# Kernel tuning notes

Measured on AMD Instinct MI355X. Metric: run time of the kernel, lower is better.

## Reference

```python
import jax, jax.numpy as jnp
import numpy as np

SR = 2  # sr_ratio

def _avgpool2x2(x):
    # x: [B,C,H,W] -> [B,C,H//2,W//2]
    B, C, H, W = x.shape
    return x.reshape(B, C, H // SR, SR, W // SR, SR).mean(axis=(3, 5))

def setup_inputs() -> dict:
    key = jax.random.key(0)
    ks = jax.random.split(key, 6)
    B, C, H, W = 8, 256, 64, 64
    d = C // 8
    sc_qk = 1.0 / np.sqrt(C)
    return {
        "x": jax.random.normal(ks[0], (B, C, H, W), jnp.float32),
        "wq": jax.random.normal(ks[1], (d, C), jnp.float32) * sc_qk,
        "wk": jax.random.normal(ks[2], (d, C), jnp.float32) * sc_qk,
        "wv": jax.random.normal(ks[3], (C, C), jnp.float32) * sc_qk,
        "wo": jax.random.normal(ks[4], (C, C), jnp.float32) * sc_qk,
        "gamma": jax.random.normal(ks[5], (1,), jnp.float32),
    }

def reference(x, wq, wk, wv, wo, gamma):
    B, C, H, W = x.shape
    N = H * W
    d = wq.shape[0]
    # q: conv1x1 then flatten+transpose -> [B, N, d]
    q = jnp.einsum('dc,bchw->bhwd', wq, x).reshape(B, N, d)
    # spatial reduction of K/V source
    x_kv = _avgpool2x2(x)
    Hk, Wk = x_kv.shape[2], x_kv.shape[3]
    Nk = Hk * Wk
    k = jnp.einsum('dc,bchw->bdhw', wk, x_kv).reshape(B, d, Nk)   # [B,d,Nk]
    v = jnp.einsum('oc,bchw->bohw', wv, x_kv).reshape(B, C, Nk)   # [B,C,Nk]
    # attn = softmax(q @ k / sqrt(d)) over Nk
    attn = jax.nn.softmax(jnp.einsum('bnd,bdm->bnm', q, k) / jnp.sqrt(jnp.float32(d)), axis=-1)
    # out = v @ attn^T -> [B,C,N]
    out = jnp.einsum('bcm,bnm->bcn', v, attn).reshape(B, C, H, W)
    out = jnp.einsum('oc,bchw->bohw', wo, out)
    return x + gamma[0] * out
```

## Files before the change

### kernel.cpp

```cpp
#include <hip/hip_runtime.h>

#define BB 8
#define CC 256
#define NN 4096
#define DD 32
#define NK 1024

typedef unsigned short u16;
typedef unsigned int   u32;
typedef __attribute__((ext_vector_type(8))) short bf16x8;
typedef __attribute__((ext_vector_type(4))) float f32x4;

#define MFMA16 __builtin_amdgcn_mfma_f32_16x16x32_bf16

#define OFF_WVO  0u
#define OFF_WQB  32768u
#define OFF_WKB  36864u
#define OFF_QF   40960u
#define OFF_KF   565248u
#define OFF_VOF  696320u

__device__ __forceinline__ u16 f2bf(float f) {
    u32 u = __float_as_uint(f);
    u += 0x7FFFu + ((u >> 16) & 1u);
    return (u16)(u >> 16);
}

__device__ __forceinline__ u32 cvt_pk_bf16(float lo, float hi) {
    u32 r;
    asm("v_cvt_pk_bf16_f32 %0, %1, %2" : "=v"(r) : "v"(lo), "v"(hi));
    return r;
}

__launch_bounds__(1024)
__global__ void wprep_kernel(const float* __restrict__ wq, const float* __restrict__ wk,
                             const float* __restrict__ wv, const float* __restrict__ wo,
                             u16* __restrict__ wqb, u16* __restrict__ wkb,
                             u16* __restrict__ wvob) {
    __shared__ float part[4][256];
    int o = blockIdx.x, t = threadIdx.x;
    int jq = t >> 8, c = t & 255;
    const float* wvp = wv + (size_t)(jq * 64) * CC + c;
    const float* wop = wo + o * CC + jq * 64;
    float acc = 0.f;
#pragma unroll 8
    for (int i = 0; i < 64; ++i)
        acc += wop[i] * wvp[(size_t)i * CC];
    part[jq][c] = acc;
    __syncthreads();
    if (t < 256)
        wvob[o * CC + t] = f2bf(part[0][t] + part[1][t] + part[2][t] + part[3][t]);
    if (o < 8) {
        const float QS = 0.17677669529663687f * 1.4426950408889634f;
        int id = o * 1024 + t;
        wqb[id] = f2bf(wq[id] * QS);
    } else if (o < 16) {
        int id = (o - 8) * 1024 + t;
        wkb[id] = f2bf(wk[id]);
    }
}

__launch_bounds__(256)
__global__ void proj_kernel(const float* __restrict__ x,
                            const u16* __restrict__ wqb, const u16* __restrict__ wkb,
                            const u16* __restrict__ wvob,
                            u16* __restrict__ qF, u16* __restrict__ kF,
                            u16* __restrict__ voF) {
    int t = threadIdx.x, w = t >> 6, l = t & 63, l15 = l & 15, lg = l >> 4;
    const f32x4 fz = {0.f, 0.f, 0.f, 0.f};

    if (blockIdx.x < 256) {
        __shared__ float xl[64 * 136];
        int b = blockIdx.x & 7, nb = blockIdx.x >> 3;
        int n0 = nb * 128;
        f32x4 acc[2][2];
        acc[0][0] = fz; acc[0][1] = fz; acc[1][0] = fz; acc[1][1] = fz;
        int cr = t >> 2, seg = (t & 3) * 32;
        for (int ch = 0; ch < 4; ++ch) {
            int c0 = ch * 64;
            const float* xs = x + ((size_t)(b * CC + c0 + cr)) * NN + n0 + seg;
#pragma unroll
            for (int p = 0; p < 8; ++p)
                *(float4*)&xl[cr * 136 + seg + p * 4] = *(const float4*)(xs + p * 4);
            __syncthreads();
#pragma unroll
            for (int ks = 0; ks < 2; ++ks) {
                int klo = ks * 32 + lg * 8;
#pragma unroll
                for (int i = 0; i < 2; ++i) {
                    int nl = w * 32 + i * 16 + l15;
                    float f0 = xl[(klo + 0) * 136 + nl];
                    float f1 = xl[(klo + 1) * 136 + nl];
                    float f2 = xl[(klo + 2) * 136 + nl];
                    float f3 = xl[(klo + 3) * 136 + nl];
                    float f4 = xl[(klo + 4) * 136 + nl];
                    float f5 = xl[(klo + 5) * 136 + nl];
                    float f6 = xl[(klo + 6) * 136 + nl];
                    float f7 = xl[(klo + 7) * 136 + nl];
                    union { u32 u[4]; bf16x8 v; } cv;
                    cv.u[0] = cvt_pk_bf16(f0, f1);
                    cv.u[1] = cvt_pk_bf16(f2, f3);
                    cv.u[2] = cvt_pk_bf16(f4, f5);
                    cv.u[3] = cvt_pk_bf16(f6, f7);
#pragma unroll
                    for (int dt = 0; dt < 2; ++dt) {
                        bf16x8 bq = *(const bf16x8*)(wqb + (size_t)(dt * 16 + l15) * CC + c0 + klo);
                        acc[i][dt] = MFMA16(cv.v, bq, acc[i][dt], 0, 0, 0);
                    }
                }
            }
            __syncthreads();
        }
        u16* outp = qF + (size_t)b * 256 * 512;
#pragma unroll
        for (int i = 0; i < 2; ++i)
#pragma unroll
            for (int dt = 0; dt < 2; ++dt)
#pragma unroll
                for (int r2 = 0; r2 < 4; ++r2) {
                    int tile = nb * 8 + w * 2 + i;
                    int dhi = dt * 2 + (l15 >> 3);
                    outp[((size_t)tile * 64 + dhi * 16 + lg * 4 + r2) * 8 + (l15 & 7)]
                        = f2bf(acc[i][dt][r2]);
                }
    } else {
        __shared__ u16 pl[64 * 42];
        int blk2 = blockIdx.x - 256;
        int b = blk2 & 7, hk = blk2 >> 3;
        f32x4 acck = fz;
        f32x4 accv[2][4];
#pragma unroll
        for (int mt = 0; mt < 2; ++mt)
#pragma unroll
            for (int ot = 0; ot < 4; ++ot) accv[mt][ot] = fz;

        int cr = t >> 2, w8 = (t & 3) * 8;
        for (int ch = 0; ch < 4; ++ch) {
            int c0 = ch * 64;
            const float* xs = x + ((size_t)(b * CC + c0 + cr)) * NN + (2 * hk) * 64 + w8 * 2;
            float4 A0 = *(const float4*)(xs +  0), A1 = *(const float4*)(xs +  4);
            float4 A2 = *(const float4*)(xs +  8), A3 = *(const float4*)(xs + 12);
            float4 B0 = *(const float4*)(xs + 64), B1 = *(const float4*)(xs + 68);
            float4 B2 = *(const float4*)(xs + 72), B3 = *(const float4*)(xs + 76);
            float p0 = 0.25f * (A0.x + A0.y + B0.x + B0.y);
            float p1 = 0.25f * (A0.z + A0.w + B0.z + B0.w);
            float p2 = 0.25f * (A1.x + A1.y + B1.x + B1.y);
            float p3 = 0.25f * (A1.z + A1.w + B1.z + B1.w);
            float p4 = 0.25f * (A2.x + A2.y + B2.x + B2.y);
            float p5 = 0.25f * (A2.z + A2.w + B2.z + B2.w);
            float p6 = 0.25f * (A3.x + A3.y + B3.x + B3.y);
            float p7 = 0.25f * (A3.z + A3.w + B3.z + B3.w);
            u32* pw = (u32*)&pl[cr * 42 + w8];
            pw[0] = cvt_pk_bf16(p0, p1);
            pw[1] = cvt_pk_bf16(p2, p3);
            pw[2] = cvt_pk_bf16(p4, p5);
            pw[3] = cvt_pk_bf16(p6, p7);
            __syncthreads();
#pragma unroll
            for (int ks = 0; ks < 2; ++ks) {
                int klo = ks * 32 + lg * 8;
                bf16x8 pm[2];
#pragma unroll
                for (int mt = 0; mt < 2; ++mt) {
                    union { u16 s[8]; bf16x8 v; } cv;
#pragma unroll
                    for (int j = 0; j < 8; ++j)
                        cv.s[j] = pl[(klo + j) * 42 + mt * 16 + l15];
                    pm[mt] = cv.v;
                }
                {
                    bf16x8 bk = *(const bf16x8*)(wkb + (size_t)((w & 1) * 16 + l15) * CC + c0 + klo);
                    acck = MFMA16(pm[w >> 1], bk, acck, 0, 0, 0);
                }
#pragma unroll
                for (int ot = 0; ot < 4; ++ot) {
                    bf16x8 ao = *(const bf16x8*)(wvob + (size_t)(w * 64 + ot * 16 + l15) * CC + c0 + klo);
#pragma unroll
                    for (int mt = 0; mt < 2; ++mt)
                        accv[mt][ot] = MFMA16(ao, pm[mt], accv[mt][ot], 0, 0, 0);
                }
            }
            __syncthreads();
        }
#pragma unroll
        for (int r2 = 0; r2 < 4; ++r2)
            kF[((size_t)(b * 64 + hk * 2 + (w >> 1)) * 64
                + ((w & 1) * 2 + (l15 >> 3)) * 16 + lg * 4 + r2) * 8 + (l15 & 7)]
                = f2bf(acck[r2]);
#pragma unroll
        for (int mt = 0; mt < 2; ++mt)
#pragma unroll
            for (int ot = 0; ot < 4; ++ot)
#pragma unroll
                for (int r2 = 0; r2 < 4; ++r2)
                    voF[(((size_t)(b * 32 + hk) * 16 + w * 4 + ot) * 64
                         + (mt * 2 + (l15 >> 3)) * 16 + lg * 4 + r2) * 8 + (l15 & 7)]
                        = f2bf(accv[mt][ot][r2]);
    }
}

__launch_bounds__(512, 4)
__global__ void attn_kernel(const u16* __restrict__ qF, const u16* __restrict__ kF,
                            const u16* __restrict__ voF, const float* __restrict__ x,
                            const float* __restrict__ gamma, float* __restrict__ out) {
    __shared__ __align__(16) u16   p_lds[2][2][64 * 40];
    __shared__ __align__(16) float rs_lds[2][64];

    const int t   = threadIdx.x;
    const int wv  = t >> 6, l = t & 63;
    const int wm  = wv >> 2, wo = wv & 3;
    const int l15 = l & 15, lg = l >> 4;
    const int b   = blockIdx.x & 7;
    const int n0  = (blockIdx.x >> 3) << 6;

    bf16x8 qf = *(const bf16x8*)(qF + ((size_t)(b * 256 + (n0 >> 4) + wo) * 64 + l) * 8);
    const u16* kfp = kF  + ((size_t)(b * 64 + wm * 32) * 64 + l) * 8;
    const u16* vbl = voF + ((size_t)((b * 32 + wm * 16) * 16 + wo * 4) * 64 + l) * 8;

    u16*       pwp = &p_lds[wm][0][(wo * 16 + l15) * 40 + lg * 4];
    const u16* prp = &p_lds[wm][0][l15 * 40 + lg * 8];

    f32x4 acc[4][4];
    const f32x4 fz = {0.f, 0.f, 0.f, 0.f};
#pragma unroll
    for (int j = 0; j < 4; ++j)
#pragma unroll
        for (int of = 0; of < 4; ++of) acc[j][of] = fz;
    float rs = 0.f;

    bf16x8 kf0 = *(const bf16x8*)(kfp);
    bf16x8 kf1 = *(const bf16x8*)(kfp + 512);
    {
        f32x4 c0 = MFMA16(kf0, qf, fz, 0, 0, 0);
        f32x4 c1 = MFMA16(kf1, qf, fz, 0, 0, 0);
        float e0 = __builtin_amdgcn_exp2f(c0[0]);
        float e1 = __builtin_amdgcn_exp2f(c0[1]);
        float e2 = __builtin_amdgcn_exp2f(c0[2]);
        float e3 = __builtin_amdgcn_exp2f(c0[3]);
        float e4 = __builtin_amdgcn_exp2f(c1[0]);
        float e5 = __builtin_amdgcn_exp2f(c1[1]);
        float e6 = __builtin_amdgcn_exp2f(c1[2]);
        float e7 = __builtin_amdgcn_exp2f(c1[3]);
        rs += (e0 + e1 + e2 + e3) + (e4 + e5 + e6 + e7);
        uint2 pw0, pw1;
        pw0.x = cvt_pk_bf16(e0, e1);
        pw0.y = cvt_pk_bf16(e2, e3);
        pw1.x = cvt_pk_bf16(e4, e5);
        pw1.y = cvt_pk_bf16(e6, e7);
        *(uint2*)pwp        = pw0;
        *(uint2*)(pwp + 16) = pw1;
    }
    kf0 = *(const bf16x8*)(kfp + 2 * 512);
    kf1 = *(const bf16x8*)(kfp + 3 * 512);
    asm volatile("s_waitcnt lgkmcnt(0)" ::: "memory");
    __builtin_amdgcn_s_barrier();

#pragma unroll 2
    for (int i = 0; i < 16; ++i) {
        const int buf = i & 1;
        bf16x8 vof[4];
#pragma unroll
        for (int of = 0; of < 4; ++of)
            vof[of] = *(const bf16x8*)(vbl + (size_t)i * 8192 + of * 512);
        bf16x8 kn0, kn1;
        if (i < 15) {
            f32x4 c0 = MFMA16(kf0, qf, fz, 0, 0, 0);
            f32x4 c1 = MFMA16(kf1, qf, fz, 0, 0, 0);
            if (i < 14) {
                kn0 = *(const bf16x8*)(kfp + (size_t)(2 * i + 4) * 512);
                kn1 = *(const bf16x8*)(kfp + (size_t)(2 * i + 5) * 512);
            }
            float e0 = __builtin_amdgcn_exp2f(c0[0]);
            float e1 = __builtin_amdgcn_exp2f(c0[1]);
            float e2 = __builtin_amdgcn_exp2f(c0[2]);
            float e3 = __builtin_amdgcn_exp2f(c0[3]);
            float e4 = __builtin_amdgcn_exp2f(c1[0]);
            float e5 = __builtin_amdgcn_exp2f(c1[1]);
            float e6 = __builtin_amdgcn_exp2f(c1[2]);
            float e7 = __builtin_amdgcn_exp2f(c1[3]);
            rs += (e0 + e1 + e2 + e3) + (e4 + e5 + e6 + e7);
            uint2 pw0, pw1;
            pw0.x = cvt_pk_bf16(e0, e1);
            pw0.y = cvt_pk_bf16(e2, e3);
            pw1.x = cvt_pk_bf16(e4, e5);
            pw1.y = cvt_pk_bf16(e6, e7);
            u16* pw = pwp + (buf ^ 1) * 2560;
            *(uint2*)pw        = pw0;
            *(uint2*)(pw + 16) = pw1;
        }
        const u16* pr = prp + buf * 2560;
        __builtin_amdgcn_s_setprio(1);
#pragma unroll
        for (int j = 0; j < 4; ++j) {
            bf16x8 pa = *(const bf16x8*)(pr + j * 640);
#pragma unroll
            for (int of = 0; of < 4; ++of)
                acc[j][of] = MFMA16(pa, vof[of], acc[j][of], 0, 0, 0);
        }
        __builtin_amdgcn_s_setprio(0);
        asm volatile("s_waitcnt lgkmcnt(0)" ::: "memory");
        __builtin_amdgcn_s_barrier();
        kf0 = kn0; kf1 = kn1;
    }

    rs += __shfl_xor(rs, 16);
    rs += __shfl_xor(rs, 32);
    if (l < 16) rs_lds[wm][wo * 16 + l] = rs;

    __syncthreads();
    float* cbuf = (float*)p_lds;
#pragma unroll
    for (int r = 0; r < 4; ++r) {
        if (wm == 1) {
#pragma unroll
            for (int of = 0; of < 4; ++of)
                *(float4*)&cbuf[((wo * 64 + l) * 16) + of * 4] =
                    make_float4(acc[r][of][0], acc[r][of][1], acc[r][of][2], acc[r][of][3]);
        }
        __syncthreads();
        if (wm == 0) {
#pragma unroll
            for (int of = 0; of < 4; ++of) {
                float4 p = *(const float4*)&cbuf[((wo * 64 + l) * 16) + of * 4];
                acc[r][of][0] += p.x; acc[r][of][1] += p.y;
                acc[r][of][2] += p.z; acc[r][of][3] += p.w;
            }
        }
        __syncthreads();
    }

    if (wm == 0) {
        float g = gamma[0];
#pragma unroll
        for (int j = 0; j < 4; ++j) {
            float r0 = rs_lds[0][j * 16 + lg * 4 + 0] + rs_lds[1][j * 16 + lg * 4 + 0];
            float r1 = rs_lds[0][j * 16 + lg * 4 + 1] + rs_lds[1][j * 16 + lg * 4 + 1];
            float r2 = rs_lds[0][j * 16 + lg * 4 + 2] + rs_lds[1][j * 16 + lg * 4 + 2];
            float r3 = rs_lds[0][j * 16 + lg * 4 + 3] + rs_lds[1][j * 16 + lg * 4 + 3];
            float fa0 = g / r0, fa1 = g / r1, fa2 = g / r2, fa3 = g / r3;
#pragma unroll
            for (int of = 0; of < 4; ++of) {
                size_t base = ((size_t)(b * CC + wo * 64 + of * 16 + l15)) * NN
                            + n0 + j * 16 + lg * 4;
                float4 xv = *(const float4*)(x + base);
                float4 ov;
                ov.x = xv.x + acc[j][of][0] * fa0;
                ov.y = xv.y + acc[j][of][1] * fa1;
                ov.z = xv.z + acc[j][of][2] * fa2;
                ov.w = xv.w + acc[j][of][3] * fa3;
                *(float4*)(out + base) = ov;
            }
        }
    }
}

extern "C" void kernel_launch(void* const* d_in, const int* in_sizes, int n_in,
                              void* d_out, int out_size, void* d_ws, size_t ws_size,
                              hipStream_t stream) {
    const float* x     = (const float*)d_in[0];
    const float* wq    = (const float*)d_in[1];
    const float* wk    = (const float*)d_in[2];
    const float* wv    = (const float*)d_in[3];
    const float* wo    = (const float*)d_in[4];
    const float* gamma = (const float*)d_in[5];
    float* out = (float*)d_out;
    float* ws  = (float*)d_ws;

    u16* wvob = (u16*)(ws + OFF_WVO);
    u16* wqb  = (u16*)(ws + OFF_WQB);
    u16* wkb  = (u16*)(ws + OFF_WKB);
    u16* qF   = (u16*)(ws + OFF_QF);
    u16* kF   = (u16*)(ws + OFF_KF);
    u16* voF  = (u16*)(ws + OFF_VOF);

    wprep_kernel<<<dim3(256), dim3(1024), 0, stream>>>(wq, wk, wv, wo, wqb, wkb, wvob);
    proj_kernel <<<dim3(512), dim3(256),  0, stream>>>(x, wqb, wkb, wvob, qF, kF, voF);
    attn_kernel <<<dim3(512), dim3(512),  0, stream>>>(qF, kF, voF, x, gamma, out);
}
```

Measured before the change: 59.88 us.

## Drop key-dimension split in attention kernel and prefetch V fragments one step ahead

The attention kernel previously split the 1024 keys between two wave groups (512 threads) and summed partial accumulators through LDS at the end. It now runs 4 waves over all 32 key chunks, which removes the cross-group reduction and its barriers. V fragments are also loaded one iteration early in software-pipelined style. In exchange each block has half the threads and a serial loop twice as long, so less parallelism hides latency, and the extra prefetch registers may reduce occupancy.

```diff
diff --git a/kernel.cpp b/kernel.cpp
--- a/kernel.cpp
+++ b/kernel.cpp
@@ -199,26 +199,25 @@
     }
 }
 
-__launch_bounds__(512, 4)
+__launch_bounds__(256, 2)
 __global__ void attn_kernel(const u16* __restrict__ qF, const u16* __restrict__ kF,
                             const u16* __restrict__ voF, const float* __restrict__ x,
                             const float* __restrict__ gamma, float* __restrict__ out) {
-    __shared__ __align__(16) u16   p_lds[2][2][64 * 40];
-    __shared__ __align__(16) float rs_lds[2][64];
+    __shared__ __align__(16) u16   p_lds[2][64 * 40];
+    __shared__ __align__(16) float rs_lds[64];
 
     const int t   = threadIdx.x;
-    const int wv  = t >> 6, l = t & 63;
-    const int wm  = wv >> 2, wo = wv & 3;
+    const int w   = t >> 6, l = t & 63;
     const int l15 = l & 15, lg = l >> 4;
     const int b   = blockIdx.x & 7;
     const int n0  = (blockIdx.x >> 3) << 6;
 
-    bf16x8 qf = *(const bf16x8*)(qF + ((size_t)(b * 256 + (n0 >> 4) + wo) * 64 + l) * 8);
-    const u16* kfp = kF  + ((size_t)(b * 64 + wm * 32) * 64 + l) * 8;
-    const u16* vbl = voF + ((size_t)((b * 32 + wm * 16) * 16 + wo * 4) * 64 + l) * 8;
-
-    u16*       pwp = &p_lds[wm][0][(wo * 16 + l15) * 40 + lg * 4];
-    const u16* prp = &p_lds[wm][0][l15 * 40 + lg * 8];
+    bf16x8 qf = *(const bf16x8*)(qF + ((size_t)(b * 256 + (n0 >> 4) + w) * 64 + l) * 8);
+    const u16* kfp = kF  + ((size_t)(b * 64) * 64 + l) * 8;
+    const u16* vbl = voF + ((size_t)((b * 32) * 16 + w * 4) * 64 + l) * 8;
+
+    u16*       pwp = &p_lds[0][(w * 16 + l15) * 40 + lg * 4];
+    const u16* prp = &p_lds[0][l15 * 40 + lg * 8];
 
     f32x4 acc[4][4];
     const f32x4 fz = {0.f, 0.f, 0.f, 0.f};
@@ -252,21 +251,27 @@
     }
     kf0 = *(const bf16x8*)(kfp + 2 * 512);
     kf1 = *(const bf16x8*)(kfp + 3 * 512);
+    bf16x8 vof[4];
+#pragma unroll
+    for (int of = 0; of < 4; ++of)
+        vof[of] = *(const bf16x8*)(vbl + of * 512);
     asm volatile("s_waitcnt lgkmcnt(0)" ::: "memory");
     __builtin_amdgcn_s_barrier();
 
 #pragma unroll 2
-    for (int i = 0; i < 16; ++i) {
+    for (int i = 0; i < 32; ++i) {
         const int buf = i & 1;
-        bf16x8 vof[4];
-#pragma unroll
-        for (int of = 0; of < 4; ++of)
-            vof[of] = *(const bf16x8*)(vbl + (size_t)i * 8192 + of * 512);
+        bf16x8 vofn[4];
+        if (i < 31) {
+#pragma unroll
+            for (int of = 0; of < 4; ++of)
+                vofn[of] = *(const bf16x8*)(vbl + (size_t)(i + 1) * 8192 + of * 512);
+        }
         bf16x8 kn0, kn1;
-        if (i < 15) {
+        if (i < 31) {
             f32x4 c0 = MFMA16(kf0, qf, fz, 0, 0, 0);
             f32x4 c1 = MFMA16(kf1, qf, fz, 0, 0, 0);
-            if (i < 14) {
+            if (i < 30) {
                 kn0 = *(const bf16x8*)(kfp + (size_t)(2 * i + 4) * 512);
                 kn1 = *(const bf16x8*)(kfp + (size_t)(2 * i + 5) * 512);
             }
@@ -301,55 +306,34 @@
         asm volatile("s_waitcnt lgkmcnt(0)" ::: "memory");
         __builtin_amdgcn_s_barrier();
         kf0 = kn0; kf1 = kn1;
+#pragma unroll
+        for (int of = 0; of < 4; ++of) vof[of] = vofn[of];
     }
 
     rs += __shfl_xor(rs, 16);
     rs += __shfl_xor(rs, 32);
-    if (l < 16) rs_lds[wm][wo * 16 + l] = rs;
-
+    if (l < 16) rs_lds[w * 16 + l] = rs;
     __syncthreads();
-    float* cbuf = (float*)p_lds;
-#pragma unroll
-    for (int r = 0; r < 4; ++r) {
-        if (wm == 1) {
-#pragma unroll
-            for (int of = 0; of < 4; ++of)
-                *(float4*)&cbuf[((wo * 64 + l) * 16) + of * 4] =
-                    make_float4(acc[r][of][0], acc[r][of][1], acc[r][of][2], acc[r][of][3]);
-        }
-        __syncthreads();
-        if (wm == 0) {
-#pragma unroll
-            for (int of = 0; of < 4; ++of) {
-                float4 p = *(const float4*)&cbuf[((wo * 64 + l) * 16) + of * 4];
-                acc[r][of][0] += p.x; acc[r][of][1] += p.y;
-                acc[r][of][2] += p.z; acc[r][of][3] += p.w;
-            }
-        }
-        __syncthreads();
-    }
-
-    if (wm == 0) {
-        float g = gamma[0];
-#pragma unroll
-        for (int j = 0; j < 4; ++j) {
-            float r0 = rs_lds[0][j * 16 + lg * 4 + 0] + rs_lds[1][j * 16 + lg * 4 + 0];
-            float r1 = rs_lds[0][j * 16 + lg * 4 + 1] + rs_lds[1][j * 16 + lg * 4 + 1];
-            float r2 = rs_lds[0][j * 16 + lg * 4 + 2] + rs_lds[1][j * 16 + lg * 4 + 2];
-            float r3 = rs_lds[0][j * 16 + lg * 4 + 3] + rs_lds[1][j * 16 + lg * 4 + 3];
-            float fa0 = g / r0, fa1 = g / r1, fa2 = g / r2, fa3 = g / r3;
-#pragma unroll
-            for (int of = 0; of < 4; ++of) {
-                size_t base = ((size_t)(b * CC + wo * 64 + of * 16 + l15)) * NN
-                            + n0 + j * 16 + lg * 4;
-                float4 xv = *(const float4*)(x + base);
-                float4 ov;
-                ov.x = xv.x + acc[j][of][0] * fa0;
-                ov.y = xv.y + acc[j][of][1] * fa1;
-                ov.z = xv.z + acc[j][of][2] * fa2;
-                ov.w = xv.w + acc[j][of][3] * fa3;
-                *(float4*)(out + base) = ov;
-            }
+
+    float g = gamma[0];
+#pragma unroll
+    for (int j = 0; j < 4; ++j) {
+        int rbase = j * 16 + lg * 4;
+        float fa0 = g / rs_lds[rbase + 0];
+        float fa1 = g / rs_lds[rbase + 1];
+        float fa2 = g / rs_lds[rbase + 2];
+        float fa3 = g / rs_lds[rbase + 3];
+#pragma unroll
+        for (int of = 0; of < 4; ++of) {
+            size_t base = ((size_t)(b * CC + w * 64 + of * 16 + l15)) * NN
+                        + n0 + j * 16 + lg * 4;
+            float4 xv = *(const float4*)(x + base);
+            float4 ov;
+            ov.x = xv.x + acc[j][of][0] * fa0;
+            ov.y = xv.y + acc[j][of][1] * fa1;
+            ov.z = xv.z + acc[j][of][2] * fa2;
+            ov.w = xv.w + acc[j][of][3] * fa3;
+            *(float4*)(out + base) = ov;
         }
     }
 }
@@ -375,5 +359,5 @@
 
     wprep_kernel<<<dim3(256), dim3(1024), 0, stream>>>(wq, wk, wv, wo, wqb, wkb, wvob);
     proj_kernel <<<dim3(512), dim3(256),  0, stream>>>(x, wqb, wkb, wvob, qF, kF, voF);
-    attn_kernel <<<dim3(512), dim3(512),  0, stream>>>(qF, kF, voF, x, gamma, out);
-}
+    attn_kernel <<<dim3(512), dim3(256),  0, stream>>>(qF, kF, voF, x, gamma, out);
+}
```

After: 58.11 us. 3.0% less time.
